# Performance work log

Measured on AMD Instinct MI355X. Metric: run time of the kernel, lower is better.

## Reference

```python
import jax, jax.numpy as jnp
import numpy as np
import math

EMBED_DIM = 2048
NUM_HEADS = 16
HEAD_DIM = EMBED_DIM // NUM_HEADS
BATCH = 2
SEQ = 2048


def setup_inputs() -> dict:
    key = jax.random.key(0)
    ks = jax.random.split(key, 6)
    scale = 1.0 / math.sqrt(EMBED_DIM)
    x = jax.random.normal(ks[0], (BATCH, SEQ, EMBED_DIM), dtype=jnp.float32)
    mask = jnp.ones((BATCH, SEQ), dtype=jnp.float32)
    Wq = jax.random.normal(ks[1], (EMBED_DIM, EMBED_DIM), dtype=jnp.float32) * scale
    Wk = jax.random.normal(ks[2], (EMBED_DIM, EMBED_DIM), dtype=jnp.float32) * scale
    Wv = jax.random.normal(ks[3], (EMBED_DIM, EMBED_DIM), dtype=jnp.float32) * scale
    Wo = jax.random.normal(ks[4], (EMBED_DIM, EMBED_DIM), dtype=jnp.float32) * scale
    return {"x": x, "mask": mask, "Wq": Wq, "Wk": Wk, "Wv": Wv, "Wo": Wo}


def _rope(q, k, seq_len):
    # q, k: [B, H, S, D]
    d = q.shape[-1]
    position = jnp.arange(seq_len, dtype=jnp.float32)[:, None]          # [S,1]
    freqs = 1.0 / (10000.0 ** (jnp.arange(0, d, 2, dtype=jnp.float32) / d))  # [D/2]
    angles = position * freqs                                            # [S,D/2]
    sin = jnp.concatenate([jnp.sin(angles), jnp.sin(angles)], axis=-1)[None, None]  # [1,1,S,D]
    cos = jnp.concatenate([jnp.cos(angles), jnp.cos(angles)], axis=-1)[None, None]

    def rotate_half(t):
        t1, t2 = jnp.split(t, 2, axis=-1)
        return jnp.concatenate([-t2, t1], axis=-1)

    q = q * cos + rotate_half(q) * sin
    k = k * cos + rotate_half(k) * sin
    return q, k


def reference(x, mask, Wq, Wk, Wv, Wo):
    B, S, E = x.shape
    H, D = NUM_HEADS, HEAD_DIM
    # nn.Linear(y) = y @ W.T
    q = (x @ Wq.T).reshape(B, S, H, D).transpose(0, 2, 1, 3)  # [B,H,S,D]
    k = (x @ Wk.T).reshape(B, S, H, D).transpose(0, 2, 1, 3)
    v = (x @ Wv.T).reshape(B, S, H, D).transpose(0, 2, 1, 3)
    q, k = _rope(q, k, S)
    scores = jnp.einsum('bhqd,bhkd->bhqk', q, k) / math.sqrt(D)  # [B,H,S,S]
    # causal mask (strict upper triangle -> -inf)
    causal = jnp.triu(jnp.full((S, S), -jnp.inf, dtype=scores.dtype), k=1)
    scores = scores + causal[None, None]
    # padding mask: [B,S] -> [B,1,1,S] over keys
    scores = scores + (1.0 - mask)[:, None, None, :] * -1e9
    attn = jax.nn.softmax(scores, axis=-1)
    context = jnp.einsum('bhqk,bhkd->bhqd', attn, v)  # [B,H,S,D]
    context = context.transpose(0, 2, 1, 3).reshape(B, S, E)
    return context @ Wo.T
```

## Files before the change

### kernel.cpp

```cpp
#include <hip/hip_runtime.h>
#include <math.h>

typedef unsigned short u16;
typedef __attribute__((ext_vector_type(8))) short bf16x8;
typedef __attribute__((ext_vector_type(8))) unsigned short u16x8;
typedef __attribute__((ext_vector_type(4))) float f32x4;

#define MFMA(a, b, c) __builtin_amdgcn_mfma_f32_16x16x32_bf16((a), (b), (c), 0, 0, 0)

#define GLOAD_LDS16(g, l)                                                     \
  __builtin_amdgcn_global_load_lds(                                           \
      (const __attribute__((address_space(1))) void*)(g),                     \
      (__attribute__((address_space(3))) void*)(l), 16, 0, 0)

#define DRAIN_VMEM() asm volatile("s_waitcnt vmcnt(0)" ::: "memory")
#define FENCE_LDS()                                                            \
  do {                                                                         \
    asm volatile("s_waitcnt lgkmcnt(0)" ::: "memory");                         \
    __builtin_amdgcn_sched_barrier(0);                                         \
  } while (0)

__device__ __forceinline__ float bf2f(u16 u) {
  union { unsigned int i; float f; } x; x.i = ((unsigned int)u) << 16; return x.f;
}
__device__ __forceinline__ u16 f2bf(float f) {
  union { float f; unsigned int i; } x; x.f = f;
  unsigned int r = x.i + 0x7FFFu + ((x.i >> 16) & 1u);
  return (u16)(r >> 16);
}

__global__ __launch_bounds__(256) void probe_all(const u16* p0, const u16* p1,
                                                 const u16* p2, const u16* p3,
                                                 const u16* p4, const u16* p5,
                                                 int* __restrict__ flags) {
  const u16* ps[6] = {p0, p1, p2, p3, p4, p5};
  const u16* p = ps[blockIdx.x];
  __shared__ int cnt;
  if (threadIdx.x == 0) cnt = 0;
  __syncthreads();
  const u16 u = p[threadIdx.x * 2];
  const int e = (u >> 7) & 0xFF;
  atomicAdd(&cnt, (e >= 110 && e <= 135) ? 1 : 0);
  __syncthreads();
  if (threadIdx.x == 0) flags[blockIdx.x] = (cnt > 128) ? 1 : 0;
}

__global__ __launch_bounds__(256) void prep_all(const void* __restrict__ x_in,
                                                const void* __restrict__ wq_in,
                                                const void* __restrict__ wk_in,
                                                const void* __restrict__ wv_in,
                                                const void* __restrict__ wo_in,
                                                const void* __restrict__ mask_in,
                                                u16* __restrict__ xc,
                                                float* __restrict__ mexp,
                                                const int* __restrict__ flags) {
  const int blk = blockIdx.x;
  if (blk < 12288) {
    const int i = blk * 256 + threadIdx.x;
    const void* in; u16* out; int fi, off;
    if (i < (1 << 20)) {
      in = x_in; out = xc; fi = 0; off = i;
    } else {
      const int k = i - (1 << 20);
      const int seg = k >> 19;
      off = k & ((1 << 19) - 1);
      in = (seg == 0) ? wq_in : (seg == 1) ? wk_in : (seg == 2) ? wv_in : wo_in;
      out = xc + ((size_t)1 << 23) + ((size_t)seg << 22);
      fi = 2 + seg;
    }
    if (flags[fi]) {
      ((u16x8*)out)[off] = ((const u16x8*)in)[off];
    } else {
      const float* f = (const float*)in + (size_t)off * 8;
      u16x8 r;
#pragma unroll
      for (int j = 0; j < 8; ++j) r[j] = f2bf(f[j]);
      ((u16x8*)out)[off] = r;
    }
  } else {
    const int i = (blk - 12288) * 256 + threadIdx.x;
    const float m = flags[1] ? bf2f(((const u16*)mask_in)[i]) : ((const float*)mask_in)[i];
    mexp[i] = (1.0f - m) * -1e9f;
  }
}

__global__ __launch_bounds__(256) void gemm_bt(const u16* __restrict__ A,
                                               const u16* __restrict__ B,
                                               void* __restrict__ dst,
                                               int K, int mode) {
  __shared__ __align__(16) u16 As[2][128 * 64];
  __shared__ __align__(16) u16 Bs[2][128 * 64];
  const int tid  = threadIdx.x;
  const int wave = tid >> 6, lane = tid & 63;
  const int quad = lane >> 4, m16 = lane & 15;
  const int wm = (wave >> 1) * 64, wn = (wave & 1) * 64;
  const size_t bi = (size_t)blockIdx.y * 128;
  const size_t bj = (size_t)blockIdx.x * 128;

  f32x4 acc[4][4];
  const f32x4 fz = {0.f, 0.f, 0.f, 0.f};
#pragma unroll
  for (int i = 0; i < 4; ++i)
#pragma unroll
    for (int j = 0; j < 4; ++j) acc[i][j] = fz;

  const u16* gA[4]; const u16* gB[4]; int lofs[4];
#pragma unroll
  for (int j = 0; j < 4; ++j) {
    const int t  = (wave * 4 + j) * 64 + lane;
    const int r  = t >> 3;
    const int cs = t & 7;
    const int c  = cs ^ (r & 7);
    gA[j] = A + (bi + r) * (size_t)K + c * 8;
    gB[j] = B + (bj + r) * (size_t)K + c * 8;
    lofs[j] = t * 8;
  }

#pragma unroll
  for (int j = 0; j < 4; ++j) GLOAD_LDS16(gA[j], &As[0][lofs[j]]);
#pragma unroll
  for (int j = 0; j < 4; ++j) GLOAD_LDS16(gB[j], &Bs[0][lofs[j]]);

  const int nIter = K >> 6;
  for (int it = 0; it < nIter; ++it) {
    DRAIN_VMEM();
    __syncthreads();
    if (it + 1 < nIter) {
      const int ko = (it + 1) << 6;
      const int nb = (it + 1) & 1;
#pragma unroll
      for (int j = 0; j < 4; ++j) GLOAD_LDS16(gA[j] + ko, &As[nb][lofs[j]]);
#pragma unroll
      for (int j = 0; j < 4; ++j) GLOAD_LDS16(gB[j] + ko, &Bs[nb][lofs[j]]);
    }
    const int cb = it & 1;

    bf16x8 af[2][4], bfv[2][4];
#pragma unroll
    for (int kk = 0; kk < 2; ++kk) {
#pragma unroll
      for (int mt = 0; mt < 4; ++mt) {
        const int m = wm + mt * 16 + m16;
        af[kk][mt] = *(const bf16x8*)&As[cb][m * 64 + ((kk * 4 + quad) ^ (m & 7)) * 8];
      }
#pragma unroll
      for (int nt = 0; nt < 4; ++nt) {
        const int n = wn + nt * 16 + m16;
        bfv[kk][nt] = *(const bf16x8*)&Bs[cb][n * 64 + ((kk * 4 + quad) ^ (n & 7)) * 8];
      }
    }
#pragma unroll
    for (int kk = 0; kk < 2; ++kk)
#pragma unroll
      for (int mt = 0; mt < 4; ++mt)
#pragma unroll
        for (int nt = 0; nt < 4; ++nt)
          acc[mt][nt] = MFMA(af[kk][mt], bfv[kk][nt], acc[mt][nt]);
  }

#pragma unroll
  for (int mt = 0; mt < 4; ++mt) {
#pragma unroll
    for (int nt = 0; nt < 4; ++nt) {
#pragma unroll
      for (int rg = 0; rg < 4; ++rg) {
        const int row = (int)bi + wm + mt * 16 + quad * 4 + rg;
        const int col = (int)bj + wn + nt * 16 + m16;
        const float v = acc[mt][nt][rg];
        if (mode == 2) {
          ((float*)dst)[(size_t)row * 2048 + col] = v;
        } else {
          const int band = col >> 11, lc = col & 2047;
          const int bb = row >> 11, s = row & 2047, hh = lc >> 7, dd = lc & 127;
          const size_t bandbase = (size_t)band * 8388608u;
          const size_t idx = (band == 2)
              ? bandbase + ((((size_t)bb * 16 + hh) * 128 + dd) * 2048 + s)
              : bandbase + ((((size_t)bb * 16 + hh) * 2048 + s) * 128 + dd);
          ((u16*)dst)[idx] = f2bf(v);
        }
      }
    }
  }
}

__global__ __launch_bounds__(256) void rope_kernel(u16* __restrict__ Qr,
                                                   u16* __restrict__ Kr) {
  const int tid = blockIdx.x * 256 + threadIdx.x;
  const int j  = tid & 63;
  const int s  = (tid >> 6) & 2047;
  const int bh = tid >> 17;
  const size_t base = ((size_t)bh * 2048 + s) * 128;
  const float freq = __expf(-(float)j * (9.2103403719761836f / 64.0f));
  float sn, cs;
  sincosf((float)s * freq, &sn, &cs);
  const float qs = 0.08838834764831845f;
  const float q1 = bf2f(Qr[base + j]), q2 = bf2f(Qr[base + j + 64]);
  Qr[base + j]      = f2bf((q1 * cs - q2 * sn) * qs);
  Qr[base + j + 64] = f2bf((q2 * cs + q1 * sn) * qs);
  const float k1 = bf2f(Kr[base + j]), k2 = bf2f(Kr[base + j + 64]);
  Kr[base + j]      = f2bf(k1 * cs - k2 * sn);
  Kr[base + j + 64] = f2bf(k2 * cs + k1 * sn);
}

__global__ __launch_bounds__(256, 2) void flash_attn(const u16* __restrict__ Q,
                                                     const u16* __restrict__ Kg,
                                                     const u16* __restrict__ Vg,
                                                     const float* __restrict__ mexp_g,
                                                     u16* __restrict__ ctx) {
  const int S = 2048, D = 128;
  __shared__ __align__(16) u16 Kt[2][64 * 128];
  __shared__ __align__(16) u16 Vt[128 * 64];
  __shared__ __align__(16) u16 Pt[64 * 64];
  const int tid  = threadIdx.x;
  const int wave = tid >> 6, lane = tid & 63;
  const int quad = lane >> 4, m16 = lane & 15;
  const int px = blockIdx.x >> 1;
  const int hl = blockIdx.x & 1;
  const int bh = blockIdx.y;
  const int b = bh >> 4, h = bh & 15;
  const size_t baseQK = (size_t)bh * S * D;
  const size_t baseV  = (size_t)bh * D * S;

  const u16* gK[4]; const u16* gV[4]; int lK[4], lV[4];
#pragma unroll
  for (int j = 0; j < 4; ++j) {
    const int t = (wave * 4 + j) * 64 + lane;
    {
      const int r = t >> 4, cs = t & 15;
      const int c = (cs & 8) | ((cs ^ r) & 7);
      gK[j] = Kg + baseQK + (size_t)r * D + c * 8;
      lK[j] = t * 8;
    }
    {
      const int d = t >> 3, cs = t & 7;
      const int c = cs ^ (d & 7);
      gV[j] = Vg + baseV + (size_t)d * S + c * 8;
      lV[j] = t * 8;
    }
  }

  const f32x4 fz = {0.f, 0.f, 0.f, 0.f};

  for (int pass = 0; pass < 2; ++pass) {
    const int qtile = pass ? px : 15 - px;
    const int q0 = qtile * 128 + hl * 64;
    const int ktmax = 2 * qtile + hl;

    __syncthreads();

    bf16x8 qf[4];
#pragma unroll
    for (int kb = 0; kb < 4; ++kb)
      qf[kb] = *(const bf16x8*)&Q[baseQK +
          (size_t)(q0 + wave * 16 + m16) * D + kb * 32 + quad * 8];

    float li[4] = {0.f, 0.f, 0.f, 0.f};
    f32x4 oacc[8];
#pragma unroll
    for (int dt = 0; dt < 8; ++dt) oacc[dt] = fz;

#pragma unroll
    for (int j = 0; j < 4; ++j) GLOAD_LDS16(gK[j], &Kt[0][lK[j]]);

    for (int kt = 0; kt <= ktmax; ++kt) {
      const int k0 = kt * 64;
      const int cb = kt & 1;
      DRAIN_VMEM();
      __syncthreads();

#pragma unroll
      for (int j = 0; j < 4; ++j) GLOAD_LDS16(gV[j] + k0, &Vt[lV[j]]);
      float madd[4];
#pragma unroll
      for (int nt = 0; nt < 4; ++nt)
        madd[nt] = mexp_g[b * S + k0 + nt * 16 + m16];
      if (kt < ktmax) {
#pragma unroll
        for (int j = 0; j < 4; ++j)
          GLOAD_LDS16(gK[j] + (size_t)(k0 + 64) * D, &Kt[cb ^ 1][lK[j]]);
      }

      f32x4 sacc[4];
#pragma unroll
      for (int nt = 0; nt < 4; ++nt) sacc[nt] = fz;
#pragma unroll
      for (int nt = 0; nt < 4; ++nt)
#pragma unroll
        for (int kb = 0; kb < 4; ++kb) {
          const int c = kb * 4 + quad;
          const int cs = (c & 8) | ((c ^ m16) & 7);
          bf16x8 kf = *(const bf16x8*)&Kt[cb][(nt * 16 + m16) * 128 + cs * 8];
          sacc[nt] = MFMA(qf[kb], kf, sacc[nt]);
        }

      if (kt < ktmax) { asm volatile("s_waitcnt vmcnt(4)" ::: "memory"); }
      else           { asm volatile("s_waitcnt vmcnt(0)" ::: "memory"); }
      __builtin_amdgcn_sched_barrier(0);

      const int R0   = q0 + wave * 16;
      const int prow = wave * 16 + quad * 4;
      if (k0 + 63 > R0) {
#pragma unroll
        for (int rg = 0; rg < 4; ++rg) {
          const int row = R0 + quad * 4 + rg;
          const int pr  = prow + rg;
          float ps = 0.f;
#pragma unroll
          for (int nt = 0; nt < 4; ++nt) {
            const int col = k0 + nt * 16 + m16;
            const float p = (col > row) ? 0.f : __expf(sacc[nt][rg] + madd[nt]);
            ps += p;
            const int c = nt * 2 + (m16 >> 3);
            Pt[pr * 64 + ((c ^ pr) & 7) * 8 + (m16 & 7)] = f2bf(p);
          }
          li[rg] += ps;
        }
      } else {
#pragma unroll
        for (int rg = 0; rg < 4; ++rg) {
          const int pr = prow + rg;
          float ps = 0.f;
#pragma unroll
          for (int nt = 0; nt < 4; ++nt) {
            const float p = __expf(sacc[nt][rg] + madd[nt]);
            ps += p;
            const int c = nt * 2 + (m16 >> 3);
            Pt[pr * 64 + ((c ^ pr) & 7) * 8 + (m16 & 7)] = f2bf(p);
          }
          li[rg] += ps;
        }
      }
      FENCE_LDS();

#pragma unroll
      for (int kb = 0; kb < 2; ++kb) {
        const int c = kb * 4 + quad;
        const int cs = (c ^ m16) & 7;
        bf16x8 pf = *(const bf16x8*)&Pt[(wave * 16 + m16) * 64 + cs * 8];
#pragma unroll
        for (int dt = 0; dt < 8; ++dt) {
          bf16x8 vf = *(const bf16x8*)&Vt[(dt * 16 + m16) * 64 + cs * 8];
          oacc[dt] = MFMA(pf, vf, oacc[dt]);
        }
      }
    }

#pragma unroll
    for (int rg = 0; rg < 4; ++rg) {
      float ls = li[rg];
#pragma unroll
      for (int mk = 1; mk < 16; mk <<= 1) ls += __shfl_xor(ls, mk, 64);
      const float inv = 1.0f / ls;
      const int srow = q0 + wave * 16 + quad * 4 + rg;
#pragma unroll
      for (int dt = 0; dt < 8; ++dt) {
        const int e = h * 128 + dt * 16 + m16;
        ctx[((size_t)b * S + srow) * 2048 + e] = f2bf(oacc[dt][rg] * inv);
      }
    }
  }
}

extern "C" void kernel_launch(void* const* d_in, const int* in_sizes, int n_in,
                              void* d_out, int out_size, void* d_ws, size_t ws_size,
                              hipStream_t stream) {
  (void)in_sizes; (void)n_in; (void)out_size; (void)ws_size;
  const int Bz = 2, S = 2048, E = 2048, H = 16, M = Bz * S;
  const size_t NX = (size_t)Bz * S * E;
  const size_t NW = (size_t)E * E;

  char* ws = (char*)d_ws;
  int*   flags = (int*)ws;
  float* mexp  = (float*)(ws + 256);
  u16* xc  = (u16*)(ws + 256 + 16384);
  u16* Wqc = xc + NX;
  u16* Qr  = Wqc + 4 * NW;
  u16* Kr  = Qr + NX;
  u16* Vt  = Kr + NX;
  u16* ctx = Vt + NX;
  u16* Woc = Wqc + 3 * NW;

  probe_all<<<6, 256, 0, stream>>>((const u16*)d_in[0], (const u16*)d_in[1],
                                   (const u16*)d_in[2], (const u16*)d_in[3],
                                   (const u16*)d_in[4], (const u16*)d_in[5], flags);

  prep_all<<<12304, 256, 0, stream>>>(d_in[0], d_in[2], d_in[3], d_in[4],
                                      d_in[5], d_in[1], xc, mexp, flags);

  gemm_bt<<<dim3(48, 32), 256, 0, stream>>>(xc, Wqc, Qr, E, 3);
  rope_kernel<<<(Bz * H * S * 64) / 256, 256, 0, stream>>>(Qr, Kr);
  flash_attn<<<dim3(16, Bz * H), 256, 0, stream>>>(Qr, Kr, Vt, mexp, ctx);
  gemm_bt<<<dim3(16, 32), 256, 0, stream>>>(ctx, Woc, d_out, E, 2);
}
```

Before: 418.1 us.

## Replace 128x128 GEMM with 256x256 eight-wave pipelined GEMM kernel

Replaces the 128x128-tile, 4-wave GEMM with a 256x256-tile, 8-wave kernel built from four 128x128 quadrants. Global-to-LDS staging of the next K tiles is interleaved with MFMA quadrant work, using partial vmcnt waits, barriers and s_setprio. Larger tiles raise operand reuse and cut global traffic per FLOP. The trade-off is fewer blocks: the output projection launches only 128 blocks, which may underfill the GPU, and more registers are needed for the accumulators.

```diff
diff --git a/kernel.cpp b/kernel.cpp
--- a/kernel.cpp
+++ b/kernel.cpp
@@ -84,89 +84,137 @@
   }
 }
 
-__global__ __launch_bounds__(256) void gemm_bt(const u16* __restrict__ A,
-                                               const u16* __restrict__ B,
-                                               void* __restrict__ dst,
-                                               int K, int mode) {
-  __shared__ __align__(16) u16 As[2][128 * 64];
-  __shared__ __align__(16) u16 Bs[2][128 * 64];
+#define G_STGA(SB, H, T)                                                          \
+  do {                                                                            \
+    GLOAD_LDS16(Ag + (bi + (H) * 128 + rr[0]) * (size_t)K + (T) * 64 + cc[0] * 8, \
+                &As[SB][H][lofs[0]]);                                             \
+    GLOAD_LDS16(Ag + (bi + (H) * 128 + rr[1]) * (size_t)K + (T) * 64 + cc[1] * 8, \
+                &As[SB][H][lofs[1]]);                                             \
+  } while (0)
+
+#define G_STGB(SB, H, T)                                                          \
+  do {                                                                            \
+    GLOAD_LDS16(Bg + (bj + (H) * 128 + rr[0]) * (size_t)K + (T) * 64 + cc[0] * 8, \
+                &Bs[SB][H][lofs[0]]);                                             \
+    GLOAD_LDS16(Bg + (bj + (H) * 128 + rr[1]) * (size_t)K + (T) * 64 + cc[1] * 8, \
+                &Bs[SB][H][lofs[1]]);                                             \
+  } while (0)
+
+#define G_LDA(CB, QM)                                                          \
+  do {                                                                         \
+    _Pragma("unroll") for (int mf = 0; mf < 4; ++mf)                           \
+    _Pragma("unroll") for (int kk = 0; kk < 2; ++kk) {                         \
+      const int lr = wr64 + mf * 16 + m16;                                     \
+      af[mf][kk] = *(const bf16x8*)&As[CB][QM]                                 \
+          [lr * 64 + (((kk * 4 + quad) ^ (lr & 7)) * 8)];                      \
+    }                                                                          \
+  } while (0)
+
+#define G_LDB(CB, QN)                                                          \
+  do {                                                                         \
+    _Pragma("unroll") for (int nf = 0; nf < 2; ++nf)                           \
+    _Pragma("unroll") for (int kk = 0; kk < 2; ++kk) {                         \
+      const int lr = wc32 + nf * 16 + m16;                                     \
+      bfr[nf][kk] = *(const bf16x8*)&Bs[CB][QN]                                \
+          [lr * 64 + (((kk * 4 + quad) ^ (lr & 7)) * 8)];                      \
+    }                                                                          \
+  } while (0)
+
+#define G_SYNC_MM(QM, QN)                                                      \
+  do {                                                                         \
+    __builtin_amdgcn_s_barrier();                                              \
+    asm volatile("s_waitcnt lgkmcnt(0)" ::: "memory");                         \
+    __builtin_amdgcn_sched_barrier(0);                                         \
+    __builtin_amdgcn_s_setprio(1);                                             \
+    _Pragma("unroll") for (int mf = 0; mf < 4; ++mf)                           \
+    _Pragma("unroll") for (int nf = 0; nf < 2; ++nf)                           \
+    _Pragma("unroll") for (int kk = 0; kk < 2; ++kk)                           \
+      acc[(QM) * 4 + mf][(QN) * 2 + nf] =                                      \
+          MFMA(af[mf][kk], bfr[nf][kk], acc[(QM) * 4 + mf][(QN) * 2 + nf]);    \
+    __builtin_amdgcn_s_setprio(0);                                             \
+    __builtin_amdgcn_s_barrier();                                              \
+  } while (0)
+
+__global__ __launch_bounds__(512, 2) void gemm256(const u16* __restrict__ Ag,
+                                                  const u16* __restrict__ Bg,
+                                                  void* __restrict__ dst,
+                                                  int K, int mode) {
+  __shared__ __align__(16) u16 As[2][2][128 * 64];
+  __shared__ __align__(16) u16 Bs[2][2][128 * 64];
   const int tid  = threadIdx.x;
-  const int wave = tid >> 6, lane = tid & 63;
+  const int wid  = tid >> 6, lane = tid & 63;
   const int quad = lane >> 4, m16 = lane & 15;
-  const int wm = (wave >> 1) * 64, wn = (wave & 1) * 64;
-  const size_t bi = (size_t)blockIdx.y * 128;
-  const size_t bj = (size_t)blockIdx.x * 128;
-
-  f32x4 acc[4][4];
+  const int wr64 = (wid >> 2) * 64;
+  const int wc32 = (wid & 3) * 32;
+  const size_t bi = (size_t)blockIdx.y * 256;
+  const size_t bj = (size_t)blockIdx.x * 256;
+
+  int rr[2], cc[2], lofs[2];
+#pragma unroll
+  for (int j = 0; j < 2; ++j) {
+    const int t = (wid * 2 + j) * 64 + lane;
+    rr[j]   = t >> 3;
+    cc[j]   = (t & 7) ^ (rr[j] & 7);
+    lofs[j] = t * 8;
+  }
+
+  f32x4 acc[8][4];
   const f32x4 fz = {0.f, 0.f, 0.f, 0.f};
 #pragma unroll
-  for (int i = 0; i < 4; ++i)
+  for (int i = 0; i < 8; ++i)
 #pragma unroll
     for (int j = 0; j < 4; ++j) acc[i][j] = fz;
 
-  const u16* gA[4]; const u16* gB[4]; int lofs[4];
-#pragma unroll
-  for (int j = 0; j < 4; ++j) {
-    const int t  = (wave * 4 + j) * 64 + lane;
-    const int r  = t >> 3;
-    const int cs = t & 7;
-    const int c  = cs ^ (r & 7);
-    gA[j] = A + (bi + r) * (size_t)K + c * 8;
-    gB[j] = B + (bj + r) * (size_t)K + c * 8;
-    lofs[j] = t * 8;
-  }
-
-#pragma unroll
-  for (int j = 0; j < 4; ++j) GLOAD_LDS16(gA[j], &As[0][lofs[j]]);
-#pragma unroll
-  for (int j = 0; j < 4; ++j) GLOAD_LDS16(gB[j], &Bs[0][lofs[j]]);
-
-  const int nIter = K >> 6;
-  for (int it = 0; it < nIter; ++it) {
-    DRAIN_VMEM();
-    __syncthreads();
-    if (it + 1 < nIter) {
-      const int ko = (it + 1) << 6;
-      const int nb = (it + 1) & 1;
-#pragma unroll
-      for (int j = 0; j < 4; ++j) GLOAD_LDS16(gA[j] + ko, &As[nb][lofs[j]]);
-#pragma unroll
-      for (int j = 0; j < 4; ++j) GLOAD_LDS16(gB[j] + ko, &Bs[nb][lofs[j]]);
-    }
-    const int cb = it & 1;
-
-    bf16x8 af[2][4], bfv[2][4];
-#pragma unroll
-    for (int kk = 0; kk < 2; ++kk) {
-#pragma unroll
-      for (int mt = 0; mt < 4; ++mt) {
-        const int m = wm + mt * 16 + m16;
-        af[kk][mt] = *(const bf16x8*)&As[cb][m * 64 + ((kk * 4 + quad) ^ (m & 7)) * 8];
-      }
-#pragma unroll
-      for (int nt = 0; nt < 4; ++nt) {
-        const int n = wn + nt * 16 + m16;
-        bfv[kk][nt] = *(const bf16x8*)&Bs[cb][n * 64 + ((kk * 4 + quad) ^ (n & 7)) * 8];
-      }
-    }
-#pragma unroll
-    for (int kk = 0; kk < 2; ++kk)
-#pragma unroll
-      for (int mt = 0; mt < 4; ++mt)
-#pragma unroll
-        for (int nt = 0; nt < 4; ++nt)
-          acc[mt][nt] = MFMA(af[kk][mt], bfv[kk][nt], acc[mt][nt]);
-  }
-
-#pragma unroll
-  for (int mt = 0; mt < 4; ++mt) {
-#pragma unroll
-    for (int nt = 0; nt < 4; ++nt) {
+  bf16x8 af[4][2], bfr[2][2];
+
+  G_STGB(0, 0, 0); G_STGA(0, 0, 0); G_STGA(0, 1, 0); G_STGB(0, 1, 0);
+  G_STGB(1, 0, 1); G_STGA(1, 0, 1);
+  asm volatile("s_waitcnt vmcnt(4)" ::: "memory");
+  __builtin_amdgcn_s_barrier();
+
+  const int nIter = K >> 7;
+  for (int i = 0; i < nIter; ++i) {
+    const int tb = 2 * i + 1, ta2 = 2 * i + 2, tb2 = 2 * i + 3;
+    const bool more = (i + 1 < nIter);
+    G_LDA(0, 0); G_LDB(0, 0);
+    G_STGA(1, 1, tb);
+    G_SYNC_MM(0, 0);
+    G_LDA(0, 1);
+    G_STGB(1, 1, tb);
+    G_SYNC_MM(1, 0);
+    G_LDA(0, 0); G_LDB(0, 1);
+    if (more) G_STGB(0, 0, ta2);
+    G_SYNC_MM(0, 1);
+    G_LDA(0, 1);
+    if (more) { G_STGA(0, 0, ta2);
+                asm volatile("s_waitcnt vmcnt(4)" ::: "memory"); }
+    else      { asm volatile("s_waitcnt vmcnt(0)" ::: "memory"); }
+    G_SYNC_MM(1, 1);
+    G_LDA(1, 0); G_LDB(1, 0);
+    if (more) G_STGA(0, 1, ta2);
+    G_SYNC_MM(0, 0);
+    G_LDA(1, 1);
+    if (more) G_STGB(0, 1, ta2);
+    G_SYNC_MM(1, 0);
+    G_LDA(1, 0); G_LDB(1, 1);
+    if (more) G_STGB(1, 0, tb2);
+    G_SYNC_MM(0, 1);
+    G_LDA(1, 1);
+    if (more) { G_STGA(1, 0, tb2);
+                asm volatile("s_waitcnt vmcnt(4)" ::: "memory"); }
+    else      { asm volatile("s_waitcnt vmcnt(0)" ::: "memory"); }
+    G_SYNC_MM(1, 1);
+  }
+
+#pragma unroll
+  for (int ai = 0; ai < 8; ++ai) {
+#pragma unroll
+    for (int bq = 0; bq < 4; ++bq) {
 #pragma unroll
       for (int rg = 0; rg < 4; ++rg) {
-        const int row = (int)bi + wm + mt * 16 + quad * 4 + rg;
-        const int col = (int)bj + wn + nt * 16 + m16;
-        const float v = acc[mt][nt][rg];
+        const int row = (int)bi + (ai >> 2) * 128 + wr64 + (ai & 3) * 16 + quad * 4 + rg;
+        const int col = (int)bj + (bq >> 1) * 128 + wc32 + (bq & 1) * 16 + m16;
+        const float v = acc[ai][bq][rg];
         if (mode == 2) {
           ((float*)dst)[(size_t)row * 2048 + col] = v;
         } else {
@@ -365,7 +413,7 @@
                               void* d_out, int out_size, void* d_ws, size_t ws_size,
                               hipStream_t stream) {
   (void)in_sizes; (void)n_in; (void)out_size; (void)ws_size;
-  const int Bz = 2, S = 2048, E = 2048, H = 16, M = Bz * S;
+  const int Bz = 2, S = 2048, E = 2048, H = 16;
   const size_t NX = (size_t)Bz * S * E;
   const size_t NW = (size_t)E * E;
 
@@ -387,8 +435,8 @@
   prep_all<<<12304, 256, 0, stream>>>(d_in[0], d_in[2], d_in[3], d_in[4],
                                       d_in[5], d_in[1], xc, mexp, flags);
 
-  gemm_bt<<<dim3(48, 32), 256, 0, stream>>>(xc, Wqc, Qr, E, 3);
+  gemm256<<<dim3(24, 16), 512, 0, stream>>>(xc, Wqc, Qr, E, 3);
   rope_kernel<<<(Bz * H * S * 64) / 256, 256, 0, stream>>>(Qr, Kr);
   flash_attn<<<dim3(16, Bz * H), 256, 0, stream>>>(Qr, Kr, Vt, mexp, ctx);
-  gemm_bt<<<dim3(16, 32), 256, 0, stream>>>(ctx, Woc, d_out, E, 2);
-}
+  gemm256<<<dim3(8, 16), 512, 0, stream>>>(ctx, Woc, d_out, E, 2);
+}
```

Measured after the change: 460.0 us. 1.1x slower.
